# Kernel tuning notes

Hardware: AMD Instinct MI355X
Metric: run time of the kernel (lower is better)

## Reference

```python
import jax, jax.numpy as jnp
import numpy as np

H_SP, W_SP, NUM_HEADS = 8, 8, 6  # split_size=[8,8], idx=0 -> H_sp=8, W_sp=8


def setup_inputs() -> dict:
    key = jax.random.key(0)
    k1, k2 = jax.random.split(key)
    B, H, W, C = 8, 128, 128, 192
    L = H * W
    qkv1 = jax.random.normal(k1, (3, B, L, C), dtype=jnp.float32)
    qkv2 = jax.random.normal(k2, (3, B, L, C), dtype=jnp.float32)
    return {"qkv1": qkv1, "qkv2": qkv2, "H": H, "W": W}


def _im2win(x, H, W):
    # (B, L, C) -> (B', num_heads, H_SP*W_SP, head_dim), B' = B * (H//H_SP) * (W//W_SP)
    B, L, C = x.shape
    hd = C // NUM_HEADS
    x = x.reshape(B, H // H_SP, H_SP, W // W_SP, W_SP, C)
    x = x.transpose(0, 1, 3, 2, 4, 5).reshape(-1, H_SP * W_SP, NUM_HEADS, hd)
    return x.transpose(0, 2, 1, 3)


def reference(qkv1, qkv2, H, W):
    q1, v1 = qkv1[0], qkv1[2]
    k2 = qkv2[1]
    B, L, C = q1.shape
    scale = (C // NUM_HEADS) ** -0.5
    q = _im2win(q1, H, W)  # (B', h, n, d)
    k = _im2win(k2, H, W)
    v = _im2win(v1, H, W)
    attn = jnp.einsum('whnd,whmd->whnm', q, k) * scale
    attn = jax.nn.softmax(attn, axis=-1)
    z = jnp.einsum('whnm,whmd->whnd', attn, v)  # (B', h, n, d)
    z = z.transpose(0, 2, 1, 3).reshape(-1, H_SP * W_SP, C)
    # windows2img: (B', n, C) -> (B, H, W, C)
    z = z.reshape(B, H // H_SP, W // W_SP, H_SP, W_SP, C)
    z = z.transpose(0, 1, 3, 2, 4, 5).reshape(B, H, W, C)
    return z
```

## Files before the change

### kernel.cpp

```cpp
#include <hip/hip_runtime.h>
#include <hip/hip_bf16.h>
#include <math.h>

#define BLC 25165824u

typedef __attribute__((ext_vector_type(8))) short bf16x8;
typedef __attribute__((ext_vector_type(4))) float f32x4;

__device__ __forceinline__ short f2bf(float f) {
    return __bfloat16_as_short(__float2bfloat16(f));
}

__global__ __launch_bounds__(384, 3)
void win_attn_v6(const float* __restrict__ qkv1,
                 const float* __restrict__ qkv2,
                 float* __restrict__ out)
{
    const int wid = blockIdx.x;
    const int b   = wid >> 8;
    const int wh  = (wid >> 4) & 15;
    const int ww  = wid & 15;

    const int tid  = threadIdx.x;
    const int h    = tid >> 6;
    const int lane = tid & 63;
    const int l15  = lane & 15;
    const int g    = lane >> 4;

    __shared__ __align__(16) unsigned char smem[76800];
    unsigned short (*q_s)[200] = (unsigned short (*)[200])(smem);
    unsigned short (*k_s)[200] = (unsigned short (*)[200])(smem + 25600);
    unsigned short (*v_s)[200] = (unsigned short (*)[200])(smem + 51200);
    float (*z_s)[200]          = (float (*)[200])(smem);

    const unsigned wbase = ((unsigned)b * 16384u + (unsigned)(wh * 1024 + ww * 8)) * 192u;
    const int trow = tid / 48;
    const int col  = (tid % 48) * 4;
    const unsigned toff = (unsigned)(trow * 192 + col);

    const float sc = 0.17677669529663689f;

    {
        f32x4 tq[8], tk[8], tv[8];
        #pragma unroll
        for (int r = 0; r < 8; ++r)
            tq[r] = *(const f32x4*)(qkv1 + wbase + r * 24576u + toff);
        #pragma unroll
        for (int r = 0; r < 8; ++r)
            tk[r] = *(const f32x4*)(qkv2 + BLC + wbase + r * 24576u + toff);
        #pragma unroll
        for (int r = 0; r < 8; ++r)
            tv[r] = *(const f32x4*)(qkv1 + 2 * BLC + wbase + r * 24576u + toff);

        #pragma unroll
        for (int r = 0; r < 8; ++r) {
            short4 s; s.x = f2bf(tq[r].x * sc); s.y = f2bf(tq[r].y * sc);
                      s.z = f2bf(tq[r].z * sc); s.w = f2bf(tq[r].w * sc);
            *(short4*)&q_s[r * 8 + trow][col] = s;
        }
        #pragma unroll
        for (int r = 0; r < 8; ++r) {
            short4 s; s.x = f2bf(tk[r].x); s.y = f2bf(tk[r].y);
                      s.z = f2bf(tk[r].z); s.w = f2bf(tk[r].w);
            *(short4*)&k_s[r * 8 + trow][col] = s;
        }
        #pragma unroll
        for (int r = 0; r < 8; ++r) {
            short4 s; s.x = f2bf(tv[r].x); s.y = f2bf(tv[r].y);
                      s.z = f2bf(tv[r].z); s.w = f2bf(tv[r].w);
            *(short4*)&v_s[r * 8 + trow][col] = s;
        }
    }
    __syncthreads();

    bf16x8 qf[4], kf[4];
    #pragma unroll
    for (int mt = 0; mt < 4; ++mt) {
        qf[mt] = *(const bf16x8*)&q_s[16 * mt + l15][32 * h + 8 * g];
        kf[mt] = *(const bf16x8*)&k_s[16 * mt + l15][32 * h + 8 * g];
    }
    bf16x8 vb[2][2];
    #pragma unroll
    for (int dt = 0; dt < 2; ++dt)
        #pragma unroll
        for (int kk = 0; kk < 2; ++kk)
            #pragma unroll
            for (int e = 0; e < 8; ++e)
                vb[dt][kk][e] = (short)v_s[32 * kk + 16 * (e >> 2) + 4 * g + (e & 3)]
                                         [32 * h + 16 * dt + l15];

    bf16x8 pf[4][2];
    float rsum[4] = {0.f, 0.f, 0.f, 0.f};
    #pragma unroll
    for (int kk = 0; kk < 2; ++kk) {
        #pragma unroll
        for (int half = 0; half < 2; ++half) {
            const int nt = 2 * kk + half;
            #pragma unroll
            for (int mt = 0; mt < 4; ++mt) {
                f32x4 acc = {0.f, 0.f, 0.f, 0.f};
                acc = __builtin_amdgcn_mfma_f32_16x16x32_bf16(kf[nt], qf[mt], acc, 0, 0, 0);
                #pragma unroll
                for (int j = 0; j < 4; ++j) {
                    const float p = __expf(acc[j]);
                    rsum[mt] += p;
                    pf[mt][kk][4 * half + j] = f2bf(p);
                }
            }
        }
    }

    float ir[4];
    #pragma unroll
    for (int mt = 0; mt < 4; ++mt) {
        float v = rsum[mt];
        v += __shfl_xor(v, 16);
        v += __shfl_xor(v, 32);
        ir[mt] = __builtin_amdgcn_rcpf(v);
    }

    f32x4 z[4][2];
    #pragma unroll
    for (int mt = 0; mt < 4; ++mt)
        #pragma unroll
        for (int dt = 0; dt < 2; ++dt)
            z[mt][dt] = f32x4{0.f, 0.f, 0.f, 0.f};
    #pragma unroll
    for (int kk = 0; kk < 2; ++kk)
        #pragma unroll
        for (int mt = 0; mt < 4; ++mt)
            #pragma unroll
            for (int dt = 0; dt < 2; ++dt)
                z[mt][dt] = __builtin_amdgcn_mfma_f32_16x16x32_bf16(pf[mt][kk], vb[dt][kk], z[mt][dt], 0, 0, 0);

    __syncthreads();
    #pragma unroll
    for (int mt = 0; mt < 4; ++mt) {
        #pragma unroll
        for (int j = 0; j < 4; ++j) {
            const float inv = __shfl(ir[mt], 4 * g + j);
            const int row = 16 * mt + 4 * g + j;
            z_s[row][32 * h + l15]      = z[mt][0][j] * inv;
            z_s[row][32 * h + 16 + l15] = z[mt][1][j] * inv;
        }
    }
    __syncthreads();

    #pragma unroll
    for (int r = 0; r < 8; ++r) {
        const f32x4 o = *(const f32x4*)&z_s[r * 8 + trow][col];
        __builtin_nontemporal_store(o, (f32x4*)(out + wbase + r * 24576u + toff));
    }
}

extern "C" void kernel_launch(void* const* d_in, const int* in_sizes, int n_in,
                              void* d_out, int out_size, void* d_ws, size_t ws_size,
                              hipStream_t stream)
{
    const float* qkv1 = (const float*)d_in[0];
    const float* qkv2 = (const float*)d_in[1];
    float* out = (float*)d_out;

    dim3 grid(2048);
    dim3 block(384);
    hipLaunchKernelGGL(win_attn_v6, grid, block, 0, stream, qkv1, qkv2, out);
}
```

Measured before the change: 80.64 us.

## Make blocks persistent over four windows and prefetch next window's inputs

Changes the kernel so each block handles four windows in a loop, shrinking the grid from 2048 to 512 blocks. The global loads for the next window are issued into registers before the current window's attention compute, and the bf16 conversion happens after the softmax, so memory latency overlaps with MFMA and exp work. This adds register pressure (96 floats of prefetch plus the packed shorts) and an extra barrier per iteration, and 512 blocks may underfill the device at 3 blocks per CU.

```diff
diff --git a/kernel.cpp b/kernel.cpp
--- a/kernel.cpp
+++ b/kernel.cpp
@@ -12,15 +12,10 @@
 }
 
 __global__ __launch_bounds__(384, 3)
-void win_attn_v6(const float* __restrict__ qkv1,
+void win_attn_v8(const float* __restrict__ qkv1,
                  const float* __restrict__ qkv2,
                  float* __restrict__ out)
 {
-    const int wid = blockIdx.x;
-    const int b   = wid >> 8;
-    const int wh  = (wid >> 4) & 15;
-    const int ww  = wid & 15;
-
     const int tid  = threadIdx.x;
     const int h    = tid >> 6;
     const int lane = tid & 63;
@@ -33,15 +28,22 @@
     unsigned short (*v_s)[200] = (unsigned short (*)[200])(smem + 51200);
     float (*z_s)[200]          = (float (*)[200])(smem);
 
-    const unsigned wbase = ((unsigned)b * 16384u + (unsigned)(wh * 1024 + ww * 8)) * 192u;
     const int trow = tid / 48;
     const int col  = (tid % 48) * 4;
     const unsigned toff = (unsigned)(trow * 192 + col);
-
     const float sc = 0.17677669529663689f;
 
-    {
-        f32x4 tq[8], tk[8], tv[8];
+    auto wbase_of = [&](int wid) -> unsigned {
+        const int b  = wid >> 8;
+        const int wh = (wid >> 4) & 15;
+        const int ww = wid & 15;
+        return ((unsigned)b * 16384u + (unsigned)(wh * 1024 + ww * 8)) * 192u;
+    };
+
+    f32x4 tq[8], tk[8], tv[8];
+    short4 sq[8], sk[8], sv[8];
+
+    auto issue = [&](unsigned wbase) {
         #pragma unroll
         for (int r = 0; r < 8; ++r)
             tq[r] = *(const f32x4*)(qkv1 + wbase + r * 24576u + toff);
@@ -51,105 +53,120 @@
         #pragma unroll
         for (int r = 0; r < 8; ++r)
             tv[r] = *(const f32x4*)(qkv1 + 2 * BLC + wbase + r * 24576u + toff);
-
+    };
+    auto convert = [&]() {
         #pragma unroll
         for (int r = 0; r < 8; ++r) {
-            short4 s; s.x = f2bf(tq[r].x * sc); s.y = f2bf(tq[r].y * sc);
-                      s.z = f2bf(tq[r].z * sc); s.w = f2bf(tq[r].w * sc);
-            *(short4*)&q_s[r * 8 + trow][col] = s;
+            sq[r].x = f2bf(tq[r].x * sc); sq[r].y = f2bf(tq[r].y * sc);
+            sq[r].z = f2bf(tq[r].z * sc); sq[r].w = f2bf(tq[r].w * sc);
+            sk[r].x = f2bf(tk[r].x); sk[r].y = f2bf(tk[r].y);
+            sk[r].z = f2bf(tk[r].z); sk[r].w = f2bf(tk[r].w);
+            sv[r].x = f2bf(tv[r].x); sv[r].y = f2bf(tv[r].y);
+            sv[r].z = f2bf(tv[r].z); sv[r].w = f2bf(tv[r].w);
         }
+    };
+
+    unsigned wb = wbase_of(blockIdx.x);
+    issue(wb);
+    convert();
+
+    for (int it = 0; it < 4; ++it) {
         #pragma unroll
         for (int r = 0; r < 8; ++r) {
-            short4 s; s.x = f2bf(tk[r].x); s.y = f2bf(tk[r].y);
-                      s.z = f2bf(tk[r].z); s.w = f2bf(tk[r].w);
-            *(short4*)&k_s[r * 8 + trow][col] = s;
+            *(short4*)&q_s[r * 8 + trow][col] = sq[r];
+            *(short4*)&k_s[r * 8 + trow][col] = sk[r];
+            *(short4*)&v_s[r * 8 + trow][col] = sv[r];
         }
+        __syncthreads();
+
+        bf16x8 qf[4], kf[4];
         #pragma unroll
-        for (int r = 0; r < 8; ++r) {
-            short4 s; s.x = f2bf(tv[r].x); s.y = f2bf(tv[r].y);
-                      s.z = f2bf(tv[r].z); s.w = f2bf(tv[r].w);
-            *(short4*)&v_s[r * 8 + trow][col] = s;
+        for (int mt = 0; mt < 4; ++mt) {
+            qf[mt] = *(const bf16x8*)&q_s[16 * mt + l15][32 * h + 8 * g];
+            kf[mt] = *(const bf16x8*)&k_s[16 * mt + l15][32 * h + 8 * g];
         }
-    }
-    __syncthreads();
+        bf16x8 vb[2][2];
+        #pragma unroll
+        for (int dt = 0; dt < 2; ++dt)
+            #pragma unroll
+            for (int kk = 0; kk < 2; ++kk)
+                #pragma unroll
+                for (int e = 0; e < 8; ++e)
+                    vb[dt][kk][e] = (short)v_s[32 * kk + 16 * (e >> 2) + 4 * g + (e & 3)]
+                                             [32 * h + 16 * dt + l15];
 
-    bf16x8 qf[4], kf[4];
-    #pragma unroll
-    for (int mt = 0; mt < 4; ++mt) {
-        qf[mt] = *(const bf16x8*)&q_s[16 * mt + l15][32 * h + 8 * g];
-        kf[mt] = *(const bf16x8*)&k_s[16 * mt + l15][32 * h + 8 * g];
-    }
-    bf16x8 vb[2][2];
-    #pragma unroll
-    for (int dt = 0; dt < 2; ++dt)
+        unsigned wb_next = 0;
+        if (it < 3) {
+            wb_next = wbase_of(blockIdx.x + 512 * (it + 1));
+            issue(wb_next);
+        }
+
+        bf16x8 pf[4][2];
+        float rsum[4] = {0.f, 0.f, 0.f, 0.f};
         #pragma unroll
-        for (int kk = 0; kk < 2; ++kk)
+        for (int kk = 0; kk < 2; ++kk) {
             #pragma unroll
-            for (int e = 0; e < 8; ++e)
-                vb[dt][kk][e] = (short)v_s[32 * kk + 16 * (e >> 2) + 4 * g + (e & 3)]
-                                         [32 * h + 16 * dt + l15];
-
-    bf16x8 pf[4][2];
-    float rsum[4] = {0.f, 0.f, 0.f, 0.f};
-    #pragma unroll
-    for (int kk = 0; kk < 2; ++kk) {
-        #pragma unroll
-        for (int half = 0; half < 2; ++half) {
-            const int nt = 2 * kk + half;
-            #pragma unroll
-            for (int mt = 0; mt < 4; ++mt) {
-                f32x4 acc = {0.f, 0.f, 0.f, 0.f};
-                acc = __builtin_amdgcn_mfma_f32_16x16x32_bf16(kf[nt], qf[mt], acc, 0, 0, 0);
+            for (int half = 0; half < 2; ++half) {
+                const int nt = 2 * kk + half;
                 #pragma unroll
-                for (int j = 0; j < 4; ++j) {
-                    const float p = __expf(acc[j]);
-                    rsum[mt] += p;
-                    pf[mt][kk][4 * half + j] = f2bf(p);
+                for (int mt = 0; mt < 4; ++mt) {
+                    f32x4 acc = {0.f, 0.f, 0.f, 0.f};
+                    acc = __builtin_amdgcn_mfma_f32_16x16x32_bf16(kf[nt], qf[mt], acc, 0, 0, 0);
+                    #pragma unroll
+                    for (int j = 0; j < 4; ++j) {
+                        const float p = __expf(acc[j]);
+                        rsum[mt] += p;
+                        pf[mt][kk][4 * half + j] = f2bf(p);
+                    }
                 }
             }
         }
-    }
+        float ir[4];
+        #pragma unroll
+        for (int mt = 0; mt < 4; ++mt) {
+            float v = rsum[mt];
+            v += __shfl_xor(v, 16);
+            v += __shfl_xor(v, 32);
+            ir[mt] = __builtin_amdgcn_rcpf(v);
+        }
 
-    float ir[4];
-    #pragma unroll
-    for (int mt = 0; mt < 4; ++mt) {
-        float v = rsum[mt];
-        v += __shfl_xor(v, 16);
-        v += __shfl_xor(v, 32);
-        ir[mt] = __builtin_amdgcn_rcpf(v);
-    }
+        if (it < 3) convert();
 
-    f32x4 z[4][2];
-    #pragma unroll
-    for (int mt = 0; mt < 4; ++mt)
-        #pragma unroll
-        for (int dt = 0; dt < 2; ++dt)
-            z[mt][dt] = f32x4{0.f, 0.f, 0.f, 0.f};
-    #pragma unroll
-    for (int kk = 0; kk < 2; ++kk)
+        f32x4 z[4][2];
         #pragma unroll
         for (int mt = 0; mt < 4; ++mt)
             #pragma unroll
             for (int dt = 0; dt < 2; ++dt)
-                z[mt][dt] = __builtin_amdgcn_mfma_f32_16x16x32_bf16(pf[mt][kk], vb[dt][kk], z[mt][dt], 0, 0, 0);
+                z[mt][dt] = f32x4{0.f, 0.f, 0.f, 0.f};
+        #pragma unroll
+        for (int kk = 0; kk < 2; ++kk)
+            #pragma unroll
+            for (int mt = 0; mt < 4; ++mt)
+                #pragma unroll
+                for (int dt = 0; dt < 2; ++dt)
+                    z[mt][dt] = __builtin_amdgcn_mfma_f32_16x16x32_bf16(pf[mt][kk], vb[dt][kk], z[mt][dt], 0, 0, 0);
 
-    __syncthreads();
-    #pragma unroll
-    for (int mt = 0; mt < 4; ++mt) {
+        __syncthreads();
         #pragma unroll
-        for (int j = 0; j < 4; ++j) {
-            const float inv = __shfl(ir[mt], 4 * g + j);
-            const int row = 16 * mt + 4 * g + j;
-            z_s[row][32 * h + l15]      = z[mt][0][j] * inv;
-            z_s[row][32 * h + 16 + l15] = z[mt][1][j] * inv;
+        for (int mt = 0; mt < 4; ++mt) {
+            #pragma unroll
+            for (int j = 0; j < 4; ++j) {
+                const float inv = __shfl(ir[mt], 4 * g + j);
+                const int row = 16 * mt + 4 * g + j;
+                z_s[row][32 * h + l15]      = z[mt][0][j] * inv;
+                z_s[row][32 * h + 16 + l15] = z[mt][1][j] * inv;
+            }
         }
-    }
-    __syncthreads();
+        __syncthreads();
 
-    #pragma unroll
-    for (int r = 0; r < 8; ++r) {
-        const f32x4 o = *(const f32x4*)&z_s[r * 8 + trow][col];
-        __builtin_nontemporal_store(o, (f32x4*)(out + wbase + r * 24576u + toff));
+        #pragma unroll
+        for (int r = 0; r < 8; ++r) {
+            const f32x4 o = *(const f32x4*)&z_s[r * 8 + trow][col];
+            __builtin_nontemporal_store(o, (f32x4*)(out + wb + r * 24576u + toff));
+        }
+
+        if (it < 3) __syncthreads();
+        wb = wb_next;
     }
 }
 
@@ -161,7 +178,7 @@
     const float* qkv2 = (const float*)d_in[1];
     float* out = (float*)d_out;
 
-    dim3 grid(2048);
+    dim3 grid(512);
     dim3 block(384);
-    hipLaunchKernelGGL(win_attn_v6, grid, block, 0, stream, qkv1, qkv2, out);
+    hipLaunchKernelGGL(win_attn_v8, grid, block, 0, stream, qkv1, qkv2, out);
 }
```

After: 210.5 us. 161% more time.
